# Kernel tuning notes

Measured on AMD Instinct MI355X. Metric: run time of the kernel, lower is better.

Reference implementation:

```python
import jax, jax.numpy as jnp
import numpy as np

N, C, TX, TY = 32, 256, 1024, 1024


def setup_inputs() -> dict:
    key = jax.random.key(0)
    ks = jax.random.split(key, 9)
    s = 1.0 / np.sqrt(C)
    return {
        "Q": jax.random.normal(ks[0], (N, C, TY), dtype=jnp.float32),
        "K": jax.random.normal(ks[1], (N, C, TX), dtype=jnp.float32),
        "V": jax.random.normal(ks[2], (N, C, TX), dtype=jnp.float32),
        "Wq": jax.random.normal(ks[3], (C, C), dtype=jnp.float32) * s,
        "bq": jax.random.normal(ks[4], (C,), dtype=jnp.float32) * 0.01,
        "Wk": jax.random.normal(ks[5], (C, C), dtype=jnp.float32) * s,
        "bk": jax.random.normal(ks[6], (C,), dtype=jnp.float32) * 0.01,
        "Wv": jax.random.normal(ks[7], (C, C), dtype=jnp.float32) * s,
        "bv": jax.random.normal(ks[8], (C,), dtype=jnp.float32) * 0.01,
    }


def _proj_tanh(W, b, x):
    # 1x1 conv over channels: (C_out, C_in) x (N, C_in, T) -> (N, C_out, T)
    return jnp.tanh(jnp.einsum("oc,nct->not", W, x) + b[None, :, None])


def reference(Q, K, V, Wq, bq, Wk, bk, Wv, bv):
    d_k = Q.shape[1]
    Qp = _proj_tanh(Wq, bq, Q)  # (N, C, Ty)
    Kp = _proj_tanh(Wk, bk, K)  # (N, C, Tx)
    Vp = _proj_tanh(Wv, bv, V)  # (N, C, Tx)
    scores = jnp.einsum("ncs,nct->nst", Kp, Qp) / jnp.sqrt(
        jnp.asarray(d_k, dtype=Q.dtype)
    )  # (N, Tx, Ty)
    A = jax.nn.softmax(scores, axis=1)  # softmax over Tx (dim=1)
    R = jnp.einsum("ncs,nst->nct", Vp, A)  # (N, C, Ty)
    return (R, A)
```

## Files before the change

kernel.cpp:

```cpp
#include <hip/hip_runtime.h>
#include <stdint.h>

#define N_B 32
#define C_D 256
#define T_D 1024
#define QB 32

typedef unsigned short u16;
typedef __attribute__((ext_vector_type(8))) short short8;
typedef __attribute__((ext_vector_type(4))) float f32x4;

__device__ __forceinline__ u16 f2bf(float f) {
    unsigned x = __float_as_uint(f);
    return (u16)((x + 0x7fffu + ((x >> 16) & 1u)) >> 16);
}

__device__ __forceinline__ void gld16(const void* g, void* l) {
    __builtin_amdgcn_global_load_lds(
        (const __attribute__((address_space(1))) uint32_t*)g,
        (__attribute__((address_space(3))) uint32_t*)l, 16, 0, 0);
}

__device__ __forceinline__ void comb(float& m, float& l, float m2, float l2) {
    float M = fmaxf(m, m2);
    l = l * __expf(m - M) + l2 * __expf(m2 - M);
    m = M;
}

__global__ __launch_bounds__(256) void conv_w(const float* __restrict__ w0,
                                              const float* __restrict__ w1,
                                              const float* __restrict__ w2,
                                              u16* __restrict__ o0,
                                              u16* __restrict__ o1,
                                              u16* __restrict__ o2) {
    const float* in = blockIdx.y == 0 ? w0 : (blockIdx.y == 1 ? w1 : w2);
    u16* out       = blockIdx.y == 0 ? o0 : (blockIdx.y == 1 ? o1 : o2);
    int i = blockIdx.x * 256 + threadIdx.x;
    out[i] = f2bf(in[i]);
}

__device__ __forceinline__ void stage_tr(const float* __restrict__ src,
                                         u16* __restrict__ sm,
                                         int sr2, int tt8) {
    float4 v0 = *(const float4*)(src);
    float4 v1 = *(const float4*)(src + 4);
    float4 w0 = *(const float4*)(src + T_D);
    float4 w1 = *(const float4*)(src + T_D + 4);
    float a[8] = {v0.x, v0.y, v0.z, v0.w, v1.x, v1.y, v1.z, v1.w};
    float b[8] = {w0.x, w0.y, w0.z, w0.w, w1.x, w1.y, w1.z, w1.w};
    const int kk = sr2 * 2;
#pragma unroll
    for (int j = 0; j < 8; ++j) {
        const int t  = tt8 + j;
        const int ks = kk ^ (((t >> 4) & 3) << 3);
        uint32_t pk = (uint32_t)f2bf(a[j]) | ((uint32_t)f2bf(b[j]) << 16);
        *(uint32_t*)(sm + t * 32 + ks) = pk;
    }
}

template <bool TRA, bool TRB, int EPI, bool DUAL>
__global__ __launch_bounds__(256) void gemm_t(
        const void* __restrict__ Av, const void* __restrict__ Bv,
        const float* __restrict__ bias, void* __restrict__ OutV,
        int Kdim, int ldo, long sA, long sB, long sO, float scale,
        const void* __restrict__ Av2, const void* __restrict__ Bv2,
        const float* __restrict__ bias2, void* __restrict__ Out2)
{
    __shared__ __align__(16) u16 smA[128 * 32];
    __shared__ __align__(16) u16 smB[128 * 32];

    int nb = blockIdx.z;
    if (DUAL && nb >= N_B) {
        nb -= N_B;
        Av = Av2; Bv = Bv2; bias = bias2; OutV = Out2;
    }
    const int n0 = blockIdx.x * 128;
    const int m0 = blockIdx.y * 128;
    const int tid = threadIdx.x;

    const int srow = tid >> 2;
    const int sk8  = (((tid & 3) ^ ((srow >> 1) & 3)) * 8);
    const int sr2  = tid >> 4;
    const int tt8  = (tid & 15) * 8;

    const u16* gA0 = nullptr; const u16* gA1 = nullptr;
    const float* tA = nullptr;
    if constexpr (TRA) {
        tA = (const float*)Av + (size_t)nb * sA + (size_t)(sr2 * 2) * T_D + m0 + tt8;
    } else {
        const u16* Ab = (const u16*)Av + (size_t)nb * sA;
        gA0 = Ab + (size_t)(m0 + srow) * Kdim + sk8;
        gA1 = gA0 + (size_t)64 * Kdim;
    }
    const u16* gB0 = nullptr; const u16* gB1 = nullptr;
    const float* tB = nullptr;
    if constexpr (TRB) {
        tB = (const float*)Bv + (size_t)nb * sB + (size_t)(sr2 * 2) * T_D + n0 + tt8;
    } else {
        const u16* Bb = (const u16*)Bv + (size_t)nb * sB;
        gB0 = Bb + (size_t)(n0 + srow) * Kdim + sk8;
        gB1 = gB0 + (size_t)64 * Kdim;
    }
    u16* lA0 = smA + tid * 8; u16* lA1 = smA + 2048 + tid * 8;
    u16* lB0 = smB + tid * 8; u16* lB1 = smB + 2048 + tid * 8;

    const int lane = tid & 63;
    const int w    = tid >> 6;
    const int wm   = (w >> 1) * 64;
    const int wn   = (w & 1) * 64;
    const int l15  = lane & 15;
    const int quad = lane >> 4;

    f32x4 acc[4][4];
#pragma unroll
    for (int i = 0; i < 4; ++i)
#pragma unroll
        for (int j = 0; j < 4; ++j) acc[i][j] = (f32x4){0.f, 0.f, 0.f, 0.f};

    for (int kb = 0; kb < Kdim; kb += 32) {
        if constexpr (TRA) {
            stage_tr(tA + (size_t)kb * T_D, smA, sr2, tt8);
        } else {
            gld16(gA0 + kb, lA0);
            gld16(gA1 + kb, lA1);
        }
        if constexpr (TRB) {
            stage_tr(tB + (size_t)kb * T_D, smB, sr2, tt8);
        } else {
            gld16(gB0 + kb, lB0);
            gld16(gB1 + kb, lB1);
        }
        __syncthreads();
        short8 af[4], bfr[4];
#pragma unroll
        for (int i = 0; i < 4; ++i) {
            const int ra = wm + i * 16 + l15;
            const int ca = TRA ? ((quad ^ ((ra >> 4) & 3)) * 8)
                               : ((quad ^ ((ra >> 1) & 3)) * 8);
            af[i] = *(const short8*)(smA + ra * 32 + ca);
            const int rb = wn + i * 16 + l15;
            const int cb = TRB ? ((quad ^ ((rb >> 4) & 3)) * 8)
                               : ((quad ^ ((rb >> 1) & 3)) * 8);
            bfr[i] = *(const short8*)(smB + rb * 32 + cb);
        }
#pragma unroll
        for (int mi = 0; mi < 4; ++mi)
#pragma unroll
            for (int ni = 0; ni < 4; ++ni)
                acc[mi][ni] = __builtin_amdgcn_mfma_f32_16x16x32_bf16(
                        af[mi], bfr[ni], acc[mi][ni], 0, 0, 0);
        __syncthreads();
    }

#pragma unroll
    for (int mi = 0; mi < 4; ++mi) {
        const int mb = m0 + wm + mi * 16 + quad * 4;
#pragma unroll
        for (int r = 0; r < 4; ++r) {
            const int m = mb + r;
            float bm = 0.f;
            if (EPI == 2) bm = bias[m];
#pragma unroll
            for (int ni = 0; ni < 4; ++ni) {
                const int nn = n0 + wn + ni * 16 + l15;
                float v = acc[mi][ni][r] * scale;
                if (EPI == 1) v = tanhf(v + bias[nn]);
                if (EPI == 2) v = tanhf(v + bm);
                ((u16*)OutV)[(size_t)nb * sO + (size_t)m * ldo + nn] = f2bf(v);
            }
        }
    }
}

__global__ __launch_bounds__(512, 4) void attn_fused(
        const u16* __restrict__ Kp,
        const u16* __restrict__ Qp,
        const u16* __restrict__ Vp,
        float* __restrict__ A,
        float* __restrict__ Rr)
{
    __shared__ __align__(16) u16 lds[40960];
    u16* smK = lds;
    u16* smQ = lds + 32768;
    u16* smP = lds;
    u16* smV = lds + 32768;
    float* red = (float*)(lds + 32768);

    const int bid = blockIdx.x;
    const int idx = (bid & 7) * 128 + (bid >> 3);
    const int nb  = idx >> 5;
    const int t0  = (idx & 31) * QB;

    const int tid  = threadIdx.x;
    const int lane = tid & 63;
    const int w    = tid >> 6;
    const int l15  = lane & 15;
    const int quad = lane >> 4;

    const u16* Kb = Kp + (size_t)nb * (T_D * C_D);
    const u16* Qb = Qp + (size_t)nb * (T_D * C_D);
    const u16* Vb = Vp + (size_t)nb * (C_D * T_D);
    float* Ab = A + (size_t)nb * ((size_t)T_D * T_D) + t0;
    float* Rb = Rr + (size_t)nb * (C_D * T_D) + t0;

    {
        const int tq   = tid >> 5;
        const int slot = tid & 31;
#pragma unroll
        for (int c = 0; c < 2; ++c) {
            const int tt = c * 16 + tq;
            const int chunk = slot ^ (tt & 7);
            gld16(Qb + (size_t)(t0 + tt) * C_D + chunk * 8,
                  smQ + c * 4096 + tid * 8);
        }
    }

    f32x4 acc[8][2];
#pragma unroll
    for (int i = 0; i < 8; ++i)
#pragma unroll
        for (int j = 0; j < 2; ++j) acc[i][j] = (f32x4){0.f, 0.f, 0.f, 0.f};

    __syncthreads();

    u16* smKw = smK + w * 4096;
    const u16* Kw = Kb + (size_t)(w * 128) * C_D;
    for (int kb = 0; kb < 8; ++kb) {
        asm volatile("s_waitcnt lgkmcnt(0)" ::: "memory");
#pragma unroll
        for (int c = 0; c < 8; ++c) {
            const int s  = c * 16 + (lane >> 2);
            const int ck = (lane & 3) ^ ((s >> 1) & 3);
            gld16(Kw + (size_t)s * C_D + kb * 32 + ck * 8,
                  smKw + c * 512 + lane * 8);
        }
        asm volatile("s_waitcnt vmcnt(0)" ::: "memory");
        __builtin_amdgcn_sched_barrier(0);
        short8 af[8], bq[2];
#pragma unroll
        for (int i = 0; i < 8; ++i) {
            const int sl = i * 16 + l15;
            af[i] = *(const short8*)(smKw + sl * 32 + ((quad ^ ((sl >> 1) & 3)) * 8));
        }
#pragma unroll
        for (int i = 0; i < 2; ++i) {
            const int t = i * 16 + l15;
            bq[i] = *(const short8*)(smQ + t * 256 + (((kb * 4 + quad) ^ (l15 & 7)) * 8));
        }
#pragma unroll
        for (int mi = 0; mi < 8; ++mi)
#pragma unroll
            for (int ni = 0; ni < 2; ++ni)
                acc[mi][ni] = __builtin_amdgcn_mfma_f32_16x16x32_bf16(
                        af[mi], bq[ni], acc[mi][ni], 0, 0, 0);
    }

    float pm2[2], pl2[2];
#pragma unroll
    for (int ni = 0; ni < 2; ++ni) {
        float m = -1e30f;
#pragma unroll
        for (int mi = 0; mi < 8; ++mi)
#pragma unroll
            for (int r = 0; r < 4; ++r)
                m = fmaxf(m, acc[mi][ni][r] * 0.0625f);
        float l = 0.f;
#pragma unroll
        for (int mi = 0; mi < 8; ++mi)
#pragma unroll
            for (int r = 0; r < 4; ++r)
                l += __expf(acc[mi][ni][r] * 0.0625f - m);
        float m2 = __shfl_xor(m, 16), l2 = __shfl_xor(l, 16);
        comb(m, l, m2, l2);
        m2 = __shfl_xor(m, 32); l2 = __shfl_xor(l, 32);
        comb(m, l, m2, l2);
        pm2[ni] = m; pl2[ni] = l;
    }

    __syncthreads();

    float* pmL = red;
    float* plL = red + 256;
    float* fM  = red + 512;
    float* fR  = red + 544;
    if (quad == 0) {
#pragma unroll
        for (int ni = 0; ni < 2; ++ni) {
            pmL[w * 32 + ni * 16 + l15] = pm2[ni];
            plL[w * 32 + ni * 16 + l15] = pl2[ni];
        }
    }
    __syncthreads();
    if (tid < 32) {
        float M = -1e30f;
#pragma unroll
        for (int j = 0; j < 8; ++j) M = fmaxf(M, pmL[j * 32 + tid]);
        float L = 0.f;
#pragma unroll
        for (int j = 0; j < 8; ++j)
            L += plL[j * 32 + tid] * __expf(pmL[j * 32 + tid] - M);
        fM[tid] = M;
        fR[tid] = 1.0f / L;
    }
    __syncthreads();
    float Mn[2], Rn[2];
#pragma unroll
    for (int ni = 0; ni < 2; ++ni) {
        Mn[ni] = fM[ni * 16 + l15];
        Rn[ni] = fR[ni * 16 + l15];
    }

#pragma unroll
    for (int mi = 0; mi < 8; ++mi) {
        const int sbase = w * 128 + mi * 16 + quad * 4;
        const int c4    = w * 32 + mi * 4 + quad;
        const int slot8 = c4 >> 1;
        const int half  = c4 & 1;
#pragma unroll
        for (int ni = 0; ni < 2; ++ni) {
            const int t = ni * 16 + l15;
            float a0 = __expf(acc[mi][ni][0] * 0.0625f - Mn[ni]) * Rn[ni];
            float a1 = __expf(acc[mi][ni][1] * 0.0625f - Mn[ni]) * Rn[ni];
            float a2 = __expf(acc[mi][ni][2] * 0.0625f - Mn[ni]) * Rn[ni];
            float a3 = __expf(acc[mi][ni][3] * 0.0625f - Mn[ni]) * Rn[ni];
            Ab[(size_t)(sbase + 0) * T_D + t] = a0;
            Ab[(size_t)(sbase + 1) * T_D + t] = a1;
            Ab[(size_t)(sbase + 2) * T_D + t] = a2;
            Ab[(size_t)(sbase + 3) * T_D + t] = a3;
            uint2 pk;
            pk.x = (uint32_t)f2bf(a0) | ((uint32_t)f2bf(a1) << 16);
            pk.y = (uint32_t)f2bf(a2) | ((uint32_t)f2bf(a3) << 16);
            *(uint2*)(smP + t * 1024 + (slot8 ^ (t & 7)) * 8 + half * 4) = pk;
        }
    }
    __syncthreads();

    f32x4 acc2[2][2];
#pragma unroll
    for (int i = 0; i < 2; ++i)
#pragma unroll
        for (int j = 0; j < 2; ++j) acc2[i][j] = (f32x4){0.f, 0.f, 0.f, 0.f};

    u16* smVw = smV + w * 1024;
    for (int kb = 0; kb < 32; ++kb) {
        asm volatile("s_waitcnt lgkmcnt(0)" ::: "memory");
#pragma unroll
        for (int c = 0; c < 2; ++c) {
            const int cc = w * 32 + c * 16 + (lane >> 2);
            const int ck = (lane & 3) ^ ((cc >> 1) & 3);
            gld16(Vb + (size_t)cc * T_D + kb * 32 + ck * 8,
                  smVw + c * 512 + lane * 8);
        }
        asm volatile("s_waitcnt vmcnt(0)" ::: "memory");
        __builtin_amdgcn_sched_barrier(0);
        short8 av[2], pb[2];
#pragma unroll
        for (int i = 0; i < 2; ++i) {
            const int cc = w * 32 + i * 16 + l15;
            av[i] = *(const short8*)(smV + cc * 32 + ((quad ^ ((cc >> 1) & 3)) * 8));
            const int t = i * 16 + l15;
            pb[i] = *(const short8*)(smP + t * 1024 + (((kb * 4 + quad) ^ (l15 & 7)) * 8));
        }
#pragma unroll
        for (int mi = 0; mi < 2; ++mi)
#pragma unroll
            for (int ni = 0; ni < 2; ++ni)
                acc2[mi][ni] = __builtin_amdgcn_mfma_f32_16x16x32_bf16(
                        av[mi], pb[ni], acc2[mi][ni], 0, 0, 0);
    }

#pragma unroll
    for (int mi = 0; mi < 2; ++mi) {
        const int cb = w * 32 + mi * 16 + quad * 4;
#pragma unroll
        for (int r = 0; r < 4; ++r)
#pragma unroll
            for (int ni = 0; ni < 2; ++ni)
                Rb[(size_t)(cb + r) * T_D + ni * 16 + l15] = acc2[mi][ni][r];
    }
}

__global__ __launch_bounds__(256) void cp_r(const float4* __restrict__ s,
                                            float4* __restrict__ d) {
    const int n = N_B * C_D * T_D / 4;
    int i = blockIdx.x * 256 + threadIdx.x;
    const int st = gridDim.x * 256;
    for (; i < n; i += st) d[i] = s[i];
}

extern "C" void kernel_launch(void* const* d_in, const int* in_sizes, int n_in,
                              void* d_out, int out_size, void* d_ws, size_t ws_size,
                              hipStream_t stream) {
    const float* Qf = (const float*)d_in[0];
    const float* Kf = (const float*)d_in[1];
    const float* Vf = (const float*)d_in[2];
    const float* Wq = (const float*)d_in[3];
    const float* bq = (const float*)d_in[4];
    const float* Wk = (const float*)d_in[5];
    const float* bk = (const float*)d_in[6];
    const float* Wv = (const float*)d_in[7];
    const float* bv = (const float*)d_in[8];

    float* Rout = (float*)d_out;
    float* Aout = Rout + (size_t)N_B * C_D * T_D;

    u16* QpT = (u16*)Rout;
    u16* KpT = (u16*)Rout + 8388608;
    u16* Wqb = (u16*)Aout;
    u16* Wkb = Wqb + 65536;
    u16* Wvb = Wkb + 65536;
    u16* Vp  = (u16*)d_in[0];
    float* Rscr = (float*)d_in[1];

    dim3 blk(256);
    const long sX = (long)C_D * T_D;

    conv_w<<<dim3(256, 3), blk, 0, stream>>>(Wq, Wk, Wv, Wqb, Wkb, Wvb);

    gemm_t<true, false, 1, true><<<dim3(2, 8, 2 * N_B), blk, 0, stream>>>(
            Qf, Wqb, bq, QpT, C_D, C_D, sX, 0, sX, 1.0f,
            Kf, Wkb, bk, KpT);
    gemm_t<false, true, 2, false><<<dim3(8, 2, N_B), blk, 0, stream>>>(
            Wvb, Vf, bv, Vp, C_D, T_D, 0, sX, sX, 1.0f,
            nullptr, nullptr, nullptr, nullptr);

    attn_fused<<<dim3(1024), dim3(512), 0, stream>>>(KpT, QpT, Vp, Aout, Rscr);

    cp_r<<<dim3(2048), blk, 0, stream>>>((const float4*)Rscr, (float4*)Rout);
}
```

Before: 369.3 us.

## Software-pipeline K and V tile loads through registers and use fast tanh

Replaces the synchronous global_load_lds staging of K and V tiles, which waited on vmcnt(0) every iteration, with register prefetch. The next half-tile or next tile is loaded into registers while the current one is written to LDS and fed to MFMAs, so global latency overlaps with compute. The projection epilogue also swaps tanhf for an exp plus reciprocal approximation. The cost is more VGPR pressure under launch_bounds(512,4), extra LDS store instructions, and slightly lower tanh accuracy.

```diff
diff --git a/kernel.cpp b/kernel.cpp
--- a/kernel.cpp
+++ b/kernel.cpp
@@ -19,6 +19,11 @@
     __builtin_amdgcn_global_load_lds(
         (const __attribute__((address_space(1))) uint32_t*)g,
         (__attribute__((address_space(3))) uint32_t*)l, 16, 0, 0);
+}
+
+__device__ __forceinline__ float ftanh(float x) {
+    float t = __expf(2.0f * x);
+    return 1.0f - 2.0f * __builtin_amdgcn_rcpf(t + 1.0f);
 }
 
 __device__ __forceinline__ void comb(float& m, float& l, float m2, float l2) {
@@ -164,8 +169,8 @@
             for (int ni = 0; ni < 4; ++ni) {
                 const int nn = n0 + wn + ni * 16 + l15;
                 float v = acc[mi][ni][r] * scale;
-                if (EPI == 1) v = tanhf(v + bias[nn]);
-                if (EPI == 2) v = tanhf(v + bm);
+                if (EPI == 1) v = ftanh(v + bias[nn]);
+                if (EPI == 2) v = ftanh(v + bm);
                 ((u16*)OutV)[(size_t)nb * sO + (size_t)m * ldo + nn] = f2bf(v);
             }
         }
@@ -225,34 +230,53 @@
 
     u16* smKw = smK + w * 4096;
     const u16* Kw = Kb + (size_t)(w * 128) * C_D;
+
+    uint4 pf[4];
+    auto ldKh = [&](int kb, int h) {
+#pragma unroll
+        for (int c = 0; c < 4; ++c) {
+            const int cc = h * 4 + c;
+            const int s  = cc * 16 + (lane >> 2);
+            const int ck = (lane & 3) ^ ((s >> 1) & 3);
+            pf[c] = *(const uint4*)(Kw + (size_t)s * C_D + kb * 32 + ck * 8);
+        }
+    };
+
+    ldKh(0, 0);
     for (int kb = 0; kb < 8; ++kb) {
-        asm volatile("s_waitcnt lgkmcnt(0)" ::: "memory");
-#pragma unroll
-        for (int c = 0; c < 8; ++c) {
-            const int s  = c * 16 + (lane >> 2);
-            const int ck = (lane & 3) ^ ((s >> 1) & 3);
-            gld16(Kw + (size_t)s * C_D + kb * 32 + ck * 8,
-                  smKw + c * 512 + lane * 8);
-        }
-        asm volatile("s_waitcnt vmcnt(0)" ::: "memory");
-        __builtin_amdgcn_sched_barrier(0);
-        short8 af[8], bq[2];
-#pragma unroll
-        for (int i = 0; i < 8; ++i) {
-            const int sl = i * 16 + l15;
-            af[i] = *(const short8*)(smKw + sl * 32 + ((quad ^ ((sl >> 1) & 3)) * 8));
-        }
-#pragma unroll
-        for (int i = 0; i < 2; ++i) {
-            const int t = i * 16 + l15;
-            bq[i] = *(const short8*)(smQ + t * 256 + (((kb * 4 + quad) ^ (l15 & 7)) * 8));
-        }
-#pragma unroll
-        for (int mi = 0; mi < 8; ++mi)
-#pragma unroll
-            for (int ni = 0; ni < 2; ++ni)
-                acc[mi][ni] = __builtin_amdgcn_mfma_f32_16x16x32_bf16(
-                        af[mi], bq[ni], acc[mi][ni], 0, 0, 0);
+        short8 bq0, bq1;
+        {
+#pragma unroll
+            for (int c = 0; c < 4; ++c)
+                *(uint4*)(smKw + c * 512 + lane * 8) = pf[c];
+            ldKh(kb, 1);
+            bq0 = *(const short8*)(smQ + l15 * 256 +
+                                   (((kb * 4 + quad) ^ (l15 & 7)) * 8));
+            bq1 = *(const short8*)(smQ + (16 + l15) * 256 +
+                                   (((kb * 4 + quad) ^ (l15 & 7)) * 8));
+#pragma unroll
+            for (int i = 0; i < 4; ++i) {
+                const int sl = i * 16 + l15;
+                short8 af = *(const short8*)(smKw + sl * 32 +
+                                             ((quad ^ ((sl >> 1) & 3)) * 8));
+                acc[i][0] = __builtin_amdgcn_mfma_f32_16x16x32_bf16(af, bq0, acc[i][0], 0, 0, 0);
+                acc[i][1] = __builtin_amdgcn_mfma_f32_16x16x32_bf16(af, bq1, acc[i][1], 0, 0, 0);
+            }
+        }
+        {
+#pragma unroll
+            for (int c = 0; c < 4; ++c)
+                *(uint4*)(smKw + (4 + c) * 512 + lane * 8) = pf[c];
+            if (kb < 7) ldKh(kb + 1, 0);
+#pragma unroll
+            for (int i = 4; i < 8; ++i) {
+                const int sl = i * 16 + l15;
+                short8 af = *(const short8*)(smKw + sl * 32 +
+                                             ((quad ^ ((sl >> 1) & 3)) * 8));
+                acc[i][0] = __builtin_amdgcn_mfma_f32_16x16x32_bf16(af, bq0, acc[i][0], 0, 0, 0);
+                acc[i][1] = __builtin_amdgcn_mfma_f32_16x16x32_bf16(af, bq1, acc[i][1], 0, 0, 0);
+            }
+        }
     }
 
     float pm2[2], pl2[2];
@@ -342,31 +366,49 @@
         for (int j = 0; j < 2; ++j) acc2[i][j] = (f32x4){0.f, 0.f, 0.f, 0.f};
 
     u16* smVw = smV + w * 1024;
-    for (int kb = 0; kb < 32; ++kb) {
-        asm volatile("s_waitcnt lgkmcnt(0)" ::: "memory");
+    uint4 pvA[2], pvB[2];
+    auto ldV = [&](uint4* d, int kb) {
 #pragma unroll
         for (int c = 0; c < 2; ++c) {
             const int cc = w * 32 + c * 16 + (lane >> 2);
             const int ck = (lane & 3) ^ ((cc >> 1) & 3);
-            gld16(Vb + (size_t)cc * T_D + kb * 32 + ck * 8,
-                  smVw + c * 512 + lane * 8);
-        }
-        asm volatile("s_waitcnt vmcnt(0)" ::: "memory");
-        __builtin_amdgcn_sched_barrier(0);
-        short8 av[2], pb[2];
-#pragma unroll
-        for (int i = 0; i < 2; ++i) {
-            const int cc = w * 32 + i * 16 + l15;
-            av[i] = *(const short8*)(smV + cc * 32 + ((quad ^ ((cc >> 1) & 3)) * 8));
-            const int t = i * 16 + l15;
-            pb[i] = *(const short8*)(smP + t * 1024 + (((kb * 4 + quad) ^ (l15 & 7)) * 8));
-        }
-#pragma unroll
-        for (int mi = 0; mi < 2; ++mi)
-#pragma unroll
-            for (int ni = 0; ni < 2; ++ni)
-                acc2[mi][ni] = __builtin_amdgcn_mfma_f32_16x16x32_bf16(
-                        av[mi], pb[ni], acc2[mi][ni], 0, 0, 0);
+            d[c] = *(const uint4*)(Vb + (size_t)cc * T_D + kb * 32 + ck * 8);
+        }
+    };
+    ldV(pvA, 0);
+    ldV(pvB, 1);
+    for (int kb = 0; kb < 32; kb += 2) {
+        {
+            *(uint4*)(smVw + lane * 8)       = pvA[0];
+            *(uint4*)(smVw + 512 + lane * 8) = pvA[1];
+            if (kb + 2 < 32) ldV(pvA, kb + 2);
+            const int cc0 = w * 32 + l15;
+            const int cc1 = w * 32 + 16 + l15;
+            short8 av0 = *(const short8*)(smV + cc0 * 32 + ((quad ^ ((cc0 >> 1) & 3)) * 8));
+            short8 av1 = *(const short8*)(smV + cc1 * 32 + ((quad ^ ((cc1 >> 1) & 3)) * 8));
+            short8 pb0 = *(const short8*)(smP + l15 * 1024 + (((kb * 4 + quad) ^ (l15 & 7)) * 8));
+            short8 pb1 = *(const short8*)(smP + (16 + l15) * 1024 + (((kb * 4 + quad) ^ (l15 & 7)) * 8));
+            acc2[0][0] = __builtin_amdgcn_mfma_f32_16x16x32_bf16(av0, pb0, acc2[0][0], 0, 0, 0);
+            acc2[0][1] = __builtin_amdgcn_mfma_f32_16x16x32_bf16(av0, pb1, acc2[0][1], 0, 0, 0);
+            acc2[1][0] = __builtin_amdgcn_mfma_f32_16x16x32_bf16(av1, pb0, acc2[1][0], 0, 0, 0);
+            acc2[1][1] = __builtin_amdgcn_mfma_f32_16x16x32_bf16(av1, pb1, acc2[1][1], 0, 0, 0);
+        }
+        {
+            const int ko = kb + 1;
+            *(uint4*)(smVw + lane * 8)       = pvB[0];
+            *(uint4*)(smVw + 512 + lane * 8) = pvB[1];
+            if (kb + 3 < 32) ldV(pvB, kb + 3);
+            const int cc0 = w * 32 + l15;
+            const int cc1 = w * 32 + 16 + l15;
+            short8 av0 = *(const short8*)(smV + cc0 * 32 + ((quad ^ ((cc0 >> 1) & 3)) * 8));
+            short8 av1 = *(const short8*)(smV + cc1 * 32 + ((quad ^ ((cc1 >> 1) & 3)) * 8));
+            short8 pb0 = *(const short8*)(smP + l15 * 1024 + (((ko * 4 + quad) ^ (l15 & 7)) * 8));
+            short8 pb1 = *(const short8*)(smP + (16 + l15) * 1024 + (((ko * 4 + quad) ^ (l15 & 7)) * 8));
+            acc2[0][0] = __builtin_amdgcn_mfma_f32_16x16x32_bf16(av0, pb0, acc2[0][0], 0, 0, 0);
+            acc2[0][1] = __builtin_amdgcn_mfma_f32_16x16x32_bf16(av0, pb1, acc2[0][1], 0, 0, 0);
+            acc2[1][0] = __builtin_amdgcn_mfma_f32_16x16x32_bf16(av1, pb0, acc2[1][0], 0, 0, 0);
+            acc2[1][1] = __builtin_amdgcn_mfma_f32_16x16x32_bf16(av1, pb1, acc2[1][1], 0, 0, 0);
+        }
     }
 
 #pragma unroll
```

New measurement: 437.7 us. 1.19x slower.
